# Kernel optimization log

Measured on AMD Instinct MI355X. Metric: run time of the kernel, lower is better.

Reference implementation:

```python
import jax, jax.numpy as jnp
import numpy as np

B, S, D = 32, 4096, 64          # batch, max seq len, input_dim
P, STRIDE, H = 8, 4, 512        # patch_size, patch_stride, hidden_size
T = (S - P) // STRIDE + 1       # static max token count (sample 0 has length S)
EPS = 1e-6


def setup_inputs() -> dict:
    key = jax.random.key(0)
    k1, k2, k3 = jax.random.split(key, 3)
    x = jax.random.normal(k1, (B, S, D), dtype=jnp.float32)
    lengths = jax.random.randint(k2, (B,), P, S + 1)
    lengths = lengths.at[0].set(S)  # at least one full-length sample -> max_tokens == T
    W = jax.random.normal(k3, (P * D, H), dtype=jnp.float32) / np.sqrt(P * D)
    b = jnp.zeros((H,), dtype=jnp.float32)
    scale = jnp.ones((H,), dtype=jnp.float32)  # RMSNorm scale
    return {"x": x, "lengths": lengths, "W": W, "b": b, "scale": scale}


def _patch(x, lengths):
    # number of tokens per sample: len(range(0, max(L-P+1, 1), STRIDE))
    n_tok = jnp.where(lengths >= P, (lengths - P) // STRIDE + 1, 1)  # [B]
    # gather positions for every (token, within-patch) slot
    pos = jnp.arange(T)[:, None] * STRIDE + jnp.arange(P)[None, :]   # [T, P]
    tokens = x[:, pos, :]                                            # [B, T, P, D]
    valid = (pos[None, :, :] < lengths[:, None, None]) \
          & (jnp.arange(T)[None, :, None] < n_tok[:, None, None])    # [B, T, P]
    tokens = jnp.where(valid[..., None], tokens, 0.0)
    return tokens.reshape(B, T, P * D), n_tok


def reference(x, lengths, W, b, scale):
    tokens, token_lengths = _patch(x, lengths)        # [B, T, P*D], [B]
    h = tokens @ W + b                                # proj -> [B, T, H]
    rms = jnp.sqrt(jnp.mean(h * h, axis=-1, keepdims=True) + EPS)
    hidden = h / rms * scale                          # RMSNorm
    return hidden, token_lengths, tokens
```

## Files before the change

kernel.cpp:

```cpp
#include <hip/hip_runtime.h>
#include <hip/hip_bf16.h>

constexpr int Bc = 32, Sc = 4096, Dc = 64, Pc = 8, STRIDEc = 4, Hc = 512;
constexpr int Tc = (Sc - Pc) / STRIDEc + 1;
constexpr int Kc = Pc * Dc;
constexpr float EPSc = 1e-6f;
constexpr int PITCH = 40;

typedef __bf16 bf16x8 __attribute__((ext_vector_type(8)));
typedef unsigned short ushort8 __attribute__((ext_vector_type(8)));
typedef float f32x4 __attribute__((ext_vector_type(4)));

__device__ __forceinline__ int n_tok_of(int len) {
    return (len >= Pc) ? ((len - Pc) / STRIDEc + 1) : 1;
}

__device__ __forceinline__ unsigned short f2bf(float f) {
    unsigned u = __builtin_bit_cast(unsigned, f);
    u = (u + 0x7FFFu + ((u >> 16) & 1u)) >> 16;
    return (unsigned short)u;
}

__global__ __launch_bounds__(256) void prep_kernel(
        const float* __restrict__ W, const int* __restrict__ lengths,
        unsigned short* __restrict__ Wt, float* __restrict__ out_tl) {
    __shared__ float tile[32][33];
    const int k0 = blockIdx.x * 32, n0 = blockIdx.y * 32;
    const int r = threadIdx.x >> 3, c = (threadIdx.x & 7) * 4;
    const float4 v = *(const float4*)(W + (size_t)(k0 + r) * Hc + n0 + c);
    tile[c + 0][r] = v.x;
    tile[c + 1][r] = v.y;
    tile[c + 2][r] = v.z;
    tile[c + 3][r] = v.w;
    __syncthreads();
    ushort4 o;
    o.x = f2bf(tile[r][c + 0]);
    o.y = f2bf(tile[r][c + 1]);
    o.z = f2bf(tile[r][c + 2]);
    o.w = f2bf(tile[r][c + 3]);
    *(ushort4*)(Wt + (size_t)(n0 + r) * Kc + k0 + c) = o;
    if (blockIdx.x == 0 && blockIdx.y == 0 && threadIdx.x < Bc)
        out_tl[threadIdx.x] = (float)n_tok_of(lengths[threadIdx.x]);
}

__global__ __launch_bounds__(256, 2) void fused_kernel(
        const float* __restrict__ x, const int* __restrict__ lengths,
        const unsigned short* __restrict__ Wt, const float* __restrict__ bias,
        const float* __restrict__ scale, float* __restrict__ hidden,
        float* __restrict__ tokens) {
    const int b  = blockIdx.y;
    const int t0 = blockIdx.x * 64;
    const int len = lengths[b];
    const int ntok = n_tok_of(len);

    __shared__ unsigned short As[64 * PITCH];
    __shared__ unsigned short Bs[512 * PITCH];
    __shared__ float ssbuf[4][64];
    __shared__ float rstd[64];

    const int tid  = threadIdx.x;
    const int w    = tid >> 6;
    const int lane = tid & 63;
    const int l15  = lane & 15;
    const int quad = lane >> 4;

    f32x4 acc[4][8];
#pragma unroll
    for (int mt = 0; mt < 4; ++mt)
#pragma unroll
        for (int nt = 0; nt < 8; ++nt) acc[mt][nt] = (f32x4){0.f, 0.f, 0.f, 0.f};

    const float* xb   = x + (size_t)b * (Sc * Dc);
    float*       tokb = tokens + (size_t)b * Tc * Kc;

    for (int k0 = 0; k0 < Kc; k0 += 32) {
        if (k0) __syncthreads();
#pragma unroll
        for (int it = 0; it < 2; ++it) {
            const int l = tid + it * 256;
            const int r = l >> 3;
            const int c = l & 7;
            const int t = t0 + r;
            const int kk = k0 + c * 4;
            const int p = kk >> 6;
            const int pos = t * STRIDEc + p;
            const bool tval = (t < Tc);
            float4 v = make_float4(0.f, 0.f, 0.f, 0.f);
            if (tval && t < ntok && pos < len)
                v = *(const float4*)(xb + (size_t)t * (STRIDEc * Dc) + kk);
            if (tval)
                *(float4*)(tokb + (size_t)t * Kc + kk) = v;
            ushort4 h4;
            h4.x = f2bf(v.x); h4.y = f2bf(v.y); h4.z = f2bf(v.z); h4.w = f2bf(v.w);
            *(ushort4*)(As + r * PITCH + c * 4) = h4;
        }
#pragma unroll
        for (int it = 0; it < 8; ++it) {
            const int cc = tid + it * 256;
            const int n  = cc >> 2;
            const int ko = (cc & 3) * 8;
            ushort8 v = *(const ushort8*)(Wt + (size_t)n * Kc + k0 + ko);
            *(ushort8*)(Bs + n * PITCH + ko) = v;
        }
        __syncthreads();
        bf16x8 af[4];
#pragma unroll
        for (int mt = 0; mt < 4; ++mt)
            af[mt] = __builtin_bit_cast(bf16x8,
                *(const ushort8*)(As + (mt * 16 + l15) * PITCH + quad * 8));
#pragma unroll
        for (int nt = 0; nt < 8; ++nt) {
            bf16x8 bfrag = __builtin_bit_cast(bf16x8,
                *(const ushort8*)(Bs + (w * 128 + nt * 16 + l15) * PITCH + quad * 8));
#pragma unroll
            for (int mt = 0; mt < 4; ++mt)
                acc[mt][nt] = __builtin_amdgcn_mfma_f32_16x16x32_bf16(
                    af[mt], bfrag, acc[mt][nt], 0, 0, 0);
        }
    }

    float ss[4][4];
#pragma unroll
    for (int mt = 0; mt < 4; ++mt)
#pragma unroll
        for (int rg = 0; rg < 4; ++rg) ss[mt][rg] = 0.f;

#pragma unroll
    for (int nt = 0; nt < 8; ++nt) {
        const float bv = bias[w * 128 + nt * 16 + l15];
#pragma unroll
        for (int mt = 0; mt < 4; ++mt)
#pragma unroll
            for (int rg = 0; rg < 4; ++rg) {
                float h = acc[mt][nt][rg] + bv;
                acc[mt][nt][rg] = h;
                ss[mt][rg] += h * h;
            }
    }
#pragma unroll
    for (int mt = 0; mt < 4; ++mt)
#pragma unroll
        for (int rg = 0; rg < 4; ++rg) {
            float s = ss[mt][rg];
            s += __shfl_xor(s, 1);
            s += __shfl_xor(s, 2);
            s += __shfl_xor(s, 4);
            s += __shfl_xor(s, 8);
            if (l15 == 0) ssbuf[w][mt * 16 + quad * 4 + rg] = s;
        }
    __syncthreads();
    if (tid < 64) {
        const float s = ssbuf[0][tid] + ssbuf[1][tid] + ssbuf[2][tid] + ssbuf[3][tid];
        rstd[tid] = rsqrtf(s * (1.0f / (float)Hc) + EPSc);
    }
    __syncthreads();

#pragma unroll
    for (int nt = 0; nt < 8; ++nt) {
        const int col = w * 128 + nt * 16 + l15;
        const float sv = scale[col];
#pragma unroll
        for (int mt = 0; mt < 4; ++mt)
#pragma unroll
            for (int rg = 0; rg < 4; ++rg) {
                const int rblk = mt * 16 + quad * 4 + rg;
                const int t = t0 + rblk;
                if (t < Tc)
                    hidden[((size_t)b * Tc + t) * Hc + col] =
                        acc[mt][nt][rg] * rstd[rblk] * sv;
            }
    }
}

extern "C" void kernel_launch(void* const* d_in, const int* in_sizes, int n_in,
                              void* d_out, int out_size, void* d_ws, size_t ws_size,
                              hipStream_t stream) {
    const float* x       = (const float*)d_in[0];
    const int*   lengths = (const int*)d_in[1];
    const float* W       = (const float*)d_in[2];
    const float* bias    = (const float*)d_in[3];
    const float* scale   = (const float*)d_in[4];

    const size_t BTH = (size_t)Bc * Tc * Hc;
    float* out    = (float*)d_out;
    float* hidden = out;
    float* tl     = out + BTH;
    float* tokens = out + BTH + Bc;

    unsigned short* Wt = (unsigned short*)d_ws;

    {
        dim3 grid(Hc / 32, Hc / 32);
        prep_kernel<<<grid, 256, 0, stream>>>(W, lengths, Wt, tl);
    }
    {
        dim3 grid(16, Bc);
        fused_kernel<<<grid, 256, 0, stream>>>(x, lengths, Wt, bias, scale,
                                               hidden, tokens);
    }
}
```

Before: 198.8 us.

## Prefetch next K-slab into registers, K-blocked W layout, swap MFMA operands for vector stores

```diff
diff --git a/kernel.cpp b/kernel.cpp
--- a/kernel.cpp
+++ b/kernel.cpp
@@ -38,7 +38,7 @@
     o.y = f2bf(tile[r][c + 1]);
     o.z = f2bf(tile[r][c + 2]);
     o.w = f2bf(tile[r][c + 3]);
-    *(ushort4*)(Wt + (size_t)(n0 + r) * Kc + k0 + c) = o;
+    *(ushort4*)(Wt + (size_t)blockIdx.x * (Hc * 32) + (size_t)(n0 + r) * 32 + c) = o;
     if (blockIdx.x == 0 && blockIdx.y == 0 && threadIdx.x < Bc)
         out_tl[threadIdx.x] = (float)n_tok_of(lengths[threadIdx.x]);
 }
@@ -56,7 +56,6 @@
     __shared__ unsigned short As[64 * PITCH];
     __shared__ unsigned short Bs[512 * PITCH];
     __shared__ float ssbuf[4][64];
-    __shared__ float rstd[64];
 
     const int tid  = threadIdx.x;
     const int w    = tid >> 6;
@@ -66,109 +65,130 @@
 
     f32x4 acc[4][8];
 #pragma unroll
-    for (int mt = 0; mt < 4; ++mt)
-#pragma unroll
-        for (int nt = 0; nt < 8; ++nt) acc[mt][nt] = (f32x4){0.f, 0.f, 0.f, 0.f};
+    for (int tt = 0; tt < 4; ++tt)
+#pragma unroll
+        for (int ct = 0; ct < 8; ++ct) acc[tt][ct] = (f32x4){0.f, 0.f, 0.f, 0.f};
 
     const float* xb   = x + (size_t)b * (Sc * Dc);
     float*       tokb = tokens + (size_t)b * Tc * Kc;
 
-    for (int k0 = 0; k0 < Kc; k0 += 32) {
-        if (k0) __syncthreads();
+    int   a_r[2], a_c[2];  bool a_tv[2];  const float* a_src[2];
+#pragma unroll
+    for (int it = 0; it < 2; ++it) {
+        const int l = tid + it * 256;
+        a_r[it] = l >> 3;
+        a_c[it] = (l & 7) * 4;
+        const int t = t0 + a_r[it];
+        a_tv[it] = (t < Tc);
+        a_src[it] = xb + (size_t)t * (STRIDEc * Dc);
+    }
+
+    float4  ra[2];
+    ushort8 rb[8];
+
+#pragma unroll
+    for (int it = 0; it < 2; ++it) {
+        const int t = t0 + a_r[it];
+        const int kk = a_c[it];
+        const int pos = t * STRIDEc + (kk >> 6);
+        ra[it] = make_float4(0.f, 0.f, 0.f, 0.f);
+        if (a_tv[it] && t < ntok && pos < len) ra[it] = *(const float4*)(a_src[it] + kk);
+    }
+#pragma unroll
+    for (int it = 0; it < 8; ++it)
+        rb[it] = *(const ushort8*)(Wt + (size_t)(tid + it * 256) * 8);
+
+    for (int step = 0; step < 16; ++step) {
+        const int k0 = step * 32;
+        if (step) __syncthreads();
+
 #pragma unroll
         for (int it = 0; it < 2; ++it) {
-            const int l = tid + it * 256;
-            const int r = l >> 3;
-            const int c = l & 7;
-            const int t = t0 + r;
-            const int kk = k0 + c * 4;
-            const int p = kk >> 6;
-            const int pos = t * STRIDEc + p;
-            const bool tval = (t < Tc);
-            float4 v = make_float4(0.f, 0.f, 0.f, 0.f);
-            if (tval && t < ntok && pos < len)
-                v = *(const float4*)(xb + (size_t)t * (STRIDEc * Dc) + kk);
-            if (tval)
-                *(float4*)(tokb + (size_t)t * Kc + kk) = v;
+            const float4 v = ra[it];
+            if (a_tv[it])
+                *(float4*)(tokb + (size_t)(t0 + a_r[it]) * Kc + k0 + a_c[it]) = v;
             ushort4 h4;
             h4.x = f2bf(v.x); h4.y = f2bf(v.y); h4.z = f2bf(v.z); h4.w = f2bf(v.w);
-            *(ushort4*)(As + r * PITCH + c * 4) = h4;
+            *(ushort4*)(As + a_r[it] * PITCH + a_c[it]) = h4;
         }
 #pragma unroll
         for (int it = 0; it < 8; ++it) {
             const int cc = tid + it * 256;
-            const int n  = cc >> 2;
-            const int ko = (cc & 3) * 8;
-            ushort8 v = *(const ushort8*)(Wt + (size_t)n * Kc + k0 + ko);
-            *(ushort8*)(Bs + n * PITCH + ko) = v;
+            *(ushort8*)(Bs + (cc >> 2) * PITCH + (cc & 3) * 8) = rb[it];
         }
         __syncthreads();
-        bf16x8 af[4];
-#pragma unroll
-        for (int mt = 0; mt < 4; ++mt)
-            af[mt] = __builtin_bit_cast(bf16x8,
-                *(const ushort8*)(As + (mt * 16 + l15) * PITCH + quad * 8));
-#pragma unroll
-        for (int nt = 0; nt < 8; ++nt) {
-            bf16x8 bfrag = __builtin_bit_cast(bf16x8,
-                *(const ushort8*)(Bs + (w * 128 + nt * 16 + l15) * PITCH + quad * 8));
-#pragma unroll
-            for (int mt = 0; mt < 4; ++mt)
-                acc[mt][nt] = __builtin_amdgcn_mfma_f32_16x16x32_bf16(
-                    af[mt], bfrag, acc[mt][nt], 0, 0, 0);
-        }
-    }
-
-    float ss[4][4];
-#pragma unroll
-    for (int mt = 0; mt < 4; ++mt)
-#pragma unroll
-        for (int rg = 0; rg < 4; ++rg) ss[mt][rg] = 0.f;
-
-#pragma unroll
-    for (int nt = 0; nt < 8; ++nt) {
-        const float bv = bias[w * 128 + nt * 16 + l15];
-#pragma unroll
-        for (int mt = 0; mt < 4; ++mt)
-#pragma unroll
-            for (int rg = 0; rg < 4; ++rg) {
-                float h = acc[mt][nt][rg] + bv;
-                acc[mt][nt][rg] = h;
-                ss[mt][rg] += h * h;
+
+        if (step < 15) {
+            const int kn = k0 + 32;
+#pragma unroll
+            for (int it = 0; it < 2; ++it) {
+                const int t = t0 + a_r[it];
+                const int kk = kn + a_c[it];
+                const int pos = t * STRIDEc + (kk >> 6);
+                ra[it] = make_float4(0.f, 0.f, 0.f, 0.f);
+                if (a_tv[it] && t < ntok && pos < len)
+                    ra[it] = *(const float4*)(a_src[it] + kk);
             }
-    }
-#pragma unroll
-    for (int mt = 0; mt < 4; ++mt)
-#pragma unroll
-        for (int rg = 0; rg < 4; ++rg) {
-            float s = ss[mt][rg];
-            s += __shfl_xor(s, 1);
-            s += __shfl_xor(s, 2);
-            s += __shfl_xor(s, 4);
-            s += __shfl_xor(s, 8);
-            if (l15 == 0) ssbuf[w][mt * 16 + quad * 4 + rg] = s;
-        }
+            const unsigned short* wsrc = Wt + (size_t)(step + 1) * (Hc * 32);
+#pragma unroll
+            for (int it = 0; it < 8; ++it)
+                rb[it] = *(const ushort8*)(wsrc + (size_t)(tid + it * 256) * 8);
+        }
+
+        bf16x8 btok[4];
+#pragma unroll
+        for (int tt = 0; tt < 4; ++tt)
+            btok[tt] = __builtin_bit_cast(bf16x8,
+                *(const ushort8*)(As + (tt * 16 + l15) * PITCH + quad * 8));
+#pragma unroll
+        for (int ct = 0; ct < 8; ++ct) {
+            bf16x8 aW = __builtin_bit_cast(bf16x8,
+                *(const ushort8*)(Bs + (w * 128 + ct * 16 + l15) * PITCH + quad * 8));
+#pragma unroll
+            for (int tt = 0; tt < 4; ++tt)
+                acc[tt][ct] = __builtin_amdgcn_mfma_f32_16x16x32_bf16(
+                    aW, btok[tt], acc[tt][ct], 0, 0, 0);
+        }
+    }
+
+    float ss[4] = {0.f, 0.f, 0.f, 0.f};
+#pragma unroll
+    for (int ct = 0; ct < 8; ++ct) {
+        const f32x4 b4 = *(const f32x4*)(bias + w * 128 + ct * 16 + quad * 4);
+#pragma unroll
+        for (int tt = 0; tt < 4; ++tt) {
+            f32x4 h = acc[tt][ct] + b4;
+            acc[tt][ct] = h;
+            ss[tt] += h[0] * h[0] + h[1] * h[1] + h[2] * h[2] + h[3] * h[3];
+        }
+    }
+#pragma unroll
+    for (int tt = 0; tt < 4; ++tt) {
+        float s = ss[tt];
+        s += __shfl_xor(s, 16);
+        s += __shfl_xor(s, 32);
+        if (quad == 0) ssbuf[w][tt * 16 + l15] = s;
+    }
     __syncthreads();
-    if (tid < 64) {
-        const float s = ssbuf[0][tid] + ssbuf[1][tid] + ssbuf[2][tid] + ssbuf[3][tid];
-        rstd[tid] = rsqrtf(s * (1.0f / (float)Hc) + EPSc);
-    }
-    __syncthreads();
-
-#pragma unroll
-    for (int nt = 0; nt < 8; ++nt) {
-        const int col = w * 128 + nt * 16 + l15;
-        const float sv = scale[col];
-#pragma unroll
-        for (int mt = 0; mt < 4; ++mt)
-#pragma unroll
-            for (int rg = 0; rg < 4; ++rg) {
-                const int rblk = mt * 16 + quad * 4 + rg;
-                const int t = t0 + rblk;
-                if (t < Tc)
-                    hidden[((size_t)b * Tc + t) * Hc + col] =
-                        acc[mt][nt][rg] * rstd[rblk] * sv;
+    float rstd[4];
+#pragma unroll
+    for (int tt = 0; tt < 4; ++tt) {
+        const int r = tt * 16 + l15;
+        const float tot = ssbuf[0][r] + ssbuf[1][r] + ssbuf[2][r] + ssbuf[3][r];
+        rstd[tt] = rsqrtf(tot * (1.0f / (float)Hc) + EPSc);
+    }
+#pragma unroll
+    for (int ct = 0; ct < 8; ++ct) {
+        const f32x4 s4 = *(const f32x4*)(scale + w * 128 + ct * 16 + quad * 4);
+#pragma unroll
+        for (int tt = 0; tt < 4; ++tt) {
+            const int t = t0 + tt * 16 + l15;
+            if (t < Tc) {
+                f32x4 o = acc[tt][ct] * rstd[tt] * s4;
+                *(f32x4*)(hidden + ((size_t)b * Tc + t) * Hc
+                          + w * 128 + ct * 16 + quad * 4) = o;
             }
+        }
     }
 }
 
```

After: 181.9 us. 8.5% less time.
